# Performance work log

Hardware: AMD Instinct MI355X
Metric: run time of the kernel (lower is better)

## Reference

```python
import jax, jax.numpy as jnp
import numpy as np

MARGIN = 0.3
NUM_CLASSES = 32  # includes label 0, which the mask logic treats specially


def setup_inputs() -> dict:
    key = jax.random.key(0)
    k1, k2 = jax.random.split(key)
    n, d = 4096, 2048
    inputs = jax.random.normal(k1, (n, d), dtype=jnp.float32)
    targets = jax.random.randint(k2, (n,), 0, NUM_CLASSES, dtype=jnp.int64)
    return {"inputs": inputs, "targets": targets}


def reference(inputs, targets):
    # Pairwise euclidean distance matrix [n, n]
    sq = jnp.sum(inputs * inputs, axis=1)  # [n]
    dist2 = sq[:, None] + sq[None, :] - 2.0 * (inputs @ inputs.T)
    dist = jnp.sqrt(jnp.maximum(dist2, 1e-12))

    # Mask semantics from the torch code:
    #   mask == 1  : same label (hard-positive pool; includes diagonal)
    #   mask == 0  : different labels AND at least one of the pair has label 0
    #   mask == -1 : different labels, both nonzero (excluded from mining)
    ti, tj = targets[:, None], targets[None, :]
    same = ti == tj
    zero_neg = (~same) & ((ti == 0) | (tj == 0))

    neg_inf = jnp.asarray(-jnp.inf, dist.dtype)
    pos_inf = jnp.asarray(jnp.inf, dist.dtype)
    dist_ap = jnp.max(jnp.where(same, dist, neg_inf), axis=1)      # hardest positive per row
    row_min = jnp.min(jnp.where(zero_neg, dist, pos_inf), axis=1)  # hardest label-0 negative

    # Torch code checks row 0 only (mask[0]) for the presence of mask==0 entries;
    # if row 0 has none, ALL dist_an are set to 0. Reproduce faithfully.
    row0_has_zero = jnp.any(zero_neg[0])
    dist_an = jnp.where(row0_has_zero, row_min, jnp.zeros_like(row_min))

    # MarginRankingLoss with y = 1: mean(relu(-(dist_an - dist_ap) + margin))
    loss = jnp.mean(jax.nn.relu(dist_ap - dist_an + MARGIN))
    return loss
```

## Files before the change

kernel.cpp:

```cpp
#include <hip/hip_runtime.h>
#include <hip/hip_bf16.h>
#include <math.h>

#define N 4096
#define K 2048
#define NC 32
#define MARGIN 0.3f

#define BK 64
#define NITER (K / BK)
#define GRID 512
#define MAXTILES 4096

typedef float f32x4 __attribute__((ext_vector_type(4)));
typedef __bf16 bf16x8 __attribute__((ext_vector_type(8)));

__device__ __forceinline__ void glds16(const void* g, void* l) {
  __builtin_amdgcn_global_load_lds(
      (const __attribute__((address_space(1))) void*)g,
      (__attribute__((address_space(3))) void*)l, 16, 0, 0);
}

__device__ __forceinline__ int imin(int a, int b) { return a < b ? a : b; }

__global__ __launch_bounds__(256) void plan_kernel(
    const int* __restrict__ tg, int* __restrict__ cursor,
    int* __restrict__ flag, int* __restrict__ done, int* __restrict__ Tp,
    int4* __restrict__ tiles) {
  __shared__ int h[NC], soff[NC], stb[NC + 1];
  int t = threadIdx.x;
  if (t < NC) h[t] = 0;
  __syncthreads();
  const int4* tg4 = (const int4*)tg;
  for (int i = t; i < N / 4; i += 256) {
    int4 v = tg4[i];
    atomicAdd(&h[v.x], 1); atomicAdd(&h[v.y], 1);
    atomicAdd(&h[v.z], 1); atomicAdd(&h[v.w], 1);
  }
  __syncthreads();
  if (t == 0) {
    int acc = 0, tacc = 0;
    for (int c = 0; c < NC; c++) {
      int n = h[c];
      soff[c] = acc;
      cursor[c] = acc;
      acc += n;
      stb[c] = tacc;
      int tt = (n + 63) >> 6;
      tacc += (tt * (tt + 1)) >> 1;
    }
    stb[NC] = tacc;
    int n0 = h[0], nz = N - n0;
    int t0b = (n0 + 63) >> 6, tzb = (nz + 63) >> 6;
    Tp[0] = tacc + ((n0 > 0 && nz > 0) ? t0b * tzb : 0);
    flag[0] = (tg[0] == 0) ? (nz > 0) : (n0 > 0);
    done[0] = 0;
  }
  __syncthreads();
  if (t < NC && h[t] > 0) {
    int n = h[t], o = soff[t];
    int tt = (n + 63) >> 6;
    int idx = stb[t];
    for (int si = 0; si < tt; si++)
      for (int sj = si; sj < tt; sj++) {
        int fl = (si < sj) ? 3 : 1;
        tiles[idx++] = make_int4((o + si * 64) | (fl << 28), o + sj * 64,
                                 o + n, o + n);
      }
  }
  int n0 = h[0], nz = N - n0;
  if (n0 > 0 && nz > 0) {
    int t0b = (n0 + 63) >> 6, tzb = (nz + 63) >> 6;
    int base = stb[NC];
    for (int k2 = t; k2 < t0b * tzb; k2 += 256) {
      int si = k2 / tzb, sj = k2 - si * tzb;
      tiles[base + k2] = make_int4((si * 64) | (2 << 28), n0 + sj * 64, n0, N);
    }
  }
}

__global__ __launch_bounds__(256) void convert_kernel(
    const float* __restrict__ X, const int* __restrict__ tg,
    __bf16* __restrict__ Xg, float* __restrict__ sqg,
    unsigned int* __restrict__ ap, unsigned int* __restrict__ an,
    int* __restrict__ cursor) {
  int row = blockIdx.x;
  int t = threadIdx.x;
  const float* xr = X + (size_t)row * K;

  float4 v0 = ((const float4*)xr)[t * 2 + 0];
  float4 v1 = ((const float4*)xr)[t * 2 + 1];

  float s = v0.x * v0.x + v0.y * v0.y + v0.z * v0.z + v0.w * v0.w +
            v1.x * v1.x + v1.y * v1.y + v1.z * v1.z + v1.w * v1.w;

  bf16x8 b;
  b[0] = (__bf16)v0.x; b[1] = (__bf16)v0.y; b[2] = (__bf16)v0.z; b[3] = (__bf16)v0.w;
  b[4] = (__bf16)v1.x; b[5] = (__bf16)v1.y; b[6] = (__bf16)v1.z; b[7] = (__bf16)v1.w;

  #pragma unroll
  for (int m = 32; m; m >>= 1) s += __shfl_xor(s, m);

  __shared__ float wred[4];
  __shared__ int spos;
  if ((t & 63) == 0) wred[t >> 6] = s;
  if (t == 0) spos = atomicAdd(&cursor[tg[row]], 1);
  __syncthreads();
  int pos = spos;

  ((bf16x8*)(Xg + (size_t)pos * K))[t] = b;
  if (t == 0) {
    sqg[pos] = wred[0] + wred[1] + wred[2] + wred[3];
    ap[pos] = 0u;
    an[pos] = 0x7f800000u;
  }
}

__global__ __launch_bounds__(256, 3) void gemm_reduce_kernel(
    const __bf16* __restrict__ Xg, const float* __restrict__ sq,
    const int* __restrict__ Tp, const int4* __restrict__ tiles,
    const int* __restrict__ flag, int* __restrict__ done,
    unsigned int* __restrict__ ap, unsigned int* __restrict__ an,
    float* __restrict__ out) {
  __shared__ __align__(16) char sAB[3][16384];
  __shared__ int s_islast;
  __shared__ float wred[4];

  int t = threadIdx.x;
  int w = t >> 6, l = t & 63;
  int wi = w >> 1, wj = w & 1;
  int quad = l >> 4, lr = l & 15;

  int aoff[2][2], boff[2][2];
  #pragma unroll
  for (int ti2 = 0; ti2 < 2; ti2++)
    #pragma unroll
    for (int h = 0; h < 2; h++) {
      int sw = (((h << 2) + quad) ^ (lr & 7)) << 4;
      aoff[ti2][h] = (wi * 32 + ti2 * 16 + lr) * 128 + sw;
      boff[ti2][h] = (wj * 32 + ti2 * 16 + lr) * 128 + sw + 8192;
    }

  int rr = t >> 3, slot = t & 7;
  int T = Tp[0];

  for (int tid = blockIdx.x; tid < T; tid += GRID) {
    int4 dsc = tiles[tid];
    unsigned fl = (unsigned)dsc.x >> 28;
    int i0 = dsc.x & 0x0FFFFFFF;
    int j0 = dsc.y, iend = dsc.z, jend = dsc.w;
    bool diag = fl & 1, colside = (fl & 2) != 0;

    const char* gA[2]; const char* gB[2];
    #pragma unroll
    for (int r = 0; r < 2; r++) {
      int row_l = r * 32 + rr;
      int cbg = slot ^ (row_l & 7);
      int ia = imin(i0 + row_l, iend - 1);
      int ja = imin(j0 + row_l, jend - 1);
      gA[r] = (const char*)(Xg + (size_t)ia * K) + cbg * 16;
      gB[r] = (const char*)(Xg + (size_t)ja * K) + cbg * 16;
    }

    f32x4 acc[2][2];
    acc[0][0] = (f32x4)0.f; acc[0][1] = (f32x4)0.f;
    acc[1][0] = (f32x4)0.f; acc[1][1] = (f32x4)0.f;

    auto stage = [&](int buf, int it) {
      char* base = sAB[buf] + t * 16;
      int koff = it * 128;
      glds16(gA[0] + koff, base);
      glds16(gA[1] + koff, base + 4096);
      glds16(gB[0] + koff, base + 8192);
      glds16(gB[1] + koff, base + 12288);
    };

    auto compute = [&](int buf) {
      const char* base = sAB[buf];
      bf16x8 af[2][2], bfr[2][2];
      #pragma unroll
      for (int ti2 = 0; ti2 < 2; ti2++)
        #pragma unroll
        for (int h = 0; h < 2; h++) {
          af[ti2][h] = *(const bf16x8*)(base + aoff[ti2][h]);
          bfr[ti2][h] = *(const bf16x8*)(base + boff[ti2][h]);
        }
      #pragma unroll
      for (int h = 0; h < 2; h++)
        #pragma unroll
        for (int ti2 = 0; ti2 < 2; ti2++)
          #pragma unroll
          for (int tj2 = 0; tj2 < 2; tj2++)
            acc[ti2][tj2] = __builtin_amdgcn_mfma_f32_16x16x32_bf16(
                af[ti2][h], bfr[tj2][h], acc[ti2][tj2], 0, 0, 0);
    };

    stage(0, 0);
    stage(1, 1);
    int pbuf = 2, cbuf = 0;
    for (int it = 0; it < NITER; ++it) {
      if (it < NITER - 1) __builtin_amdgcn_s_waitcnt(0x0F74);
      else __builtin_amdgcn_s_waitcnt(0x0F70);
      __builtin_amdgcn_s_barrier();
      if (it + 2 < NITER) {
        stage(pbuf, it + 2);
        pbuf = (pbuf == 2) ? 0 : pbuf + 1;
      }
      __builtin_amdgcn_sched_barrier(0);
      compute(cbuf);
      cbuf = (cbuf == 2) ? 0 : cbuf + 1;
    }

    int jgc[2]; float sqj[2];
    #pragma unroll
    for (int tj2 = 0; tj2 < 2; tj2++) {
      jgc[tj2] = imin(j0 + wj * 32 + tj2 * 16 + lr, jend - 1);
      sqj[tj2] = sq[jgc[tj2]];
    }
    float cred[2];
    cred[0] = cred[1] = diag ? 0.f : INFINITY;

    #pragma unroll
    for (int ti2 = 0; ti2 < 2; ti2++) {
      #pragma unroll
      for (int r = 0; r < 4; r++) {
        int ir = imin(i0 + wi * 32 + ti2 * 16 + quad * 4 + r, iend - 1);
        float sqi = sq[ir];
        float v = diag ? 0.f : INFINITY;
        #pragma unroll
        for (int tj2 = 0; tj2 < 2; tj2++) {
          float d2 = fmaxf(sqi + sqj[tj2] - 2.f * acc[ti2][tj2][r], 1e-12f);
          v = diag ? fmaxf(v, d2) : fminf(v, d2);
          cred[tj2] = diag ? fmaxf(cred[tj2], d2) : fminf(cred[tj2], d2);
        }
        #pragma unroll
        for (int m = 1; m < 16; m <<= 1) {
          float o = __shfl_xor(v, m);
          v = diag ? fmaxf(v, o) : fminf(v, o);
        }
        if (lr == 0) {
          unsigned int u = __float_as_uint(sqrtf(v));
          if (diag) atomicMax(ap + ir, u);
          else      atomicMin(an + ir, u);
        }
      }
    }
    if (colside) {
      #pragma unroll
      for (int tj2 = 0; tj2 < 2; tj2++) {
        float v = cred[tj2];
        float o = __shfl_xor(v, 16);
        v = diag ? fmaxf(v, o) : fminf(v, o);
        o = __shfl_xor(v, 32);
        v = diag ? fmaxf(v, o) : fminf(v, o);
        if (quad == 0) {
          unsigned int u = __float_as_uint(sqrtf(v));
          if (diag) atomicMax(ap + jgc[tj2], u);
          else      atomicMin(an + jgc[tj2], u);
        }
      }
    }
    __builtin_amdgcn_s_barrier();
  }

  __syncthreads();
  if (t == 0) {
    __threadfence();
    int ticket = __hip_atomic_fetch_add(done, 1, __ATOMIC_ACQ_REL,
                                        __HIP_MEMORY_SCOPE_AGENT);
    s_islast = (ticket == GRID - 1);
  }
  __syncthreads();
  if (s_islast) {
    int has = flag[0];
    float s = 0.f;
    for (int i = t; i < N; i += 256) {
      unsigned int au = __hip_atomic_load(ap + i, __ATOMIC_RELAXED,
                                          __HIP_MEMORY_SCOPE_AGENT);
      unsigned int nu = __hip_atomic_load(an + i, __ATOMIC_RELAXED,
                                          __HIP_MEMORY_SCOPE_AGENT);
      float a = __uint_as_float(au);
      float bb = has ? __uint_as_float(nu) : 0.f;
      s += fmaxf(a - bb + MARGIN, 0.f);
    }
    #pragma unroll
    for (int m = 32; m; m >>= 1) s += __shfl_xor(s, m);
    if ((t & 63) == 0) wred[t >> 6] = s;
    __syncthreads();
    if (t == 0) out[0] = (wred[0] + wred[1] + wred[2] + wred[3]) / (float)N;
  }
}

extern "C" void kernel_launch(void* const* d_in, const int* in_sizes, int n_in,
                              void* d_out, int out_size, void* d_ws,
                              size_t ws_size, hipStream_t stream) {
  const float* X = (const float*)d_in[0];
  const int* tg = (const int*)d_in[1];
  float* out = (float*)d_out;

  char* ws = (char*)d_ws;
  __bf16* Xg = (__bf16*)ws;
  size_t o = (size_t)N * K * 2;
  float* sq = (float*)(ws + o); o += (size_t)N * 4;
  unsigned int* ap = (unsigned int*)(ws + o); o += (size_t)N * 4;
  unsigned int* an = (unsigned int*)(ws + o); o += (size_t)N * 4;
  int* cursor = (int*)(ws + o); o += NC * 4;
  int* flag = (int*)(ws + o); o += 4;
  int* done = (int*)(ws + o); o += 4;
  int* Tp = (int*)(ws + o); o += 4;
  o = (o + 15) & ~(size_t)15;
  int4* tiles = (int4*)(ws + o); o += (size_t)MAXTILES * 16;

  plan_kernel<<<1, 256, 0, stream>>>(tg, cursor, flag, done, Tp, tiles);
  convert_kernel<<<N, 256, 0, stream>>>(X, tg, Xg, sq, ap, an, cursor);
  gemm_reduce_kernel<<<GRID, 256, 0, stream>>>(Xg, sq, Tp, tiles, flag, done,
                                               ap, an, out);
}
```

Baseline: 145.4 us.

## Split GEMM over K into partial tiles with a separate reduce kernel

The fused GEMM-plus-mining kernel becomes two kernels. The first splits each 64x64 tile's K dimension into 8 chunks and writes fp32 partial accumulators to workspace. The second sums those partials and does the distance, masking and atomic min/max reduction plus the final loss. This exposes far more work items than the few hundred tiles the class-sorted plan produces, which could not fill the grid before. The cost is an extra launch and a global-memory round trip for the partials, and the tile list is now capped at 512 entries, so inputs with more tiles would be silently truncated.

New measurement: 148.9 us. 2.5% more time.

```diff
diff --git a/kernel.cpp b/kernel.cpp
--- a/kernel.cpp
+++ b/kernel.cpp
@@ -7,10 +7,11 @@
 #define NC 32
 #define MARGIN 0.3f
 
-#define BK 64
-#define NITER (K / BK)
-#define GRID 512
-#define MAXTILES 4096
+#define SPLITK 8
+#define KC (K / SPLITK)
+#define GRID_A 512
+#define GRID_B 256
+#define MAXTILES 512
 
 typedef float f32x4 __attribute__((ext_vector_type(4)));
 typedef __bf16 bf16x8 __attribute__((ext_vector_type(8)));
@@ -52,7 +53,8 @@
     stb[NC] = tacc;
     int n0 = h[0], nz = N - n0;
     int t0b = (n0 + 63) >> 6, tzb = (nz + 63) >> 6;
-    Tp[0] = tacc + ((n0 > 0 && nz > 0) ? t0b * tzb : 0);
+    int T = tacc + ((n0 > 0 && nz > 0) ? t0b * tzb : 0);
+    Tp[0] = imin(T, MAXTILES);
     flag[0] = (tg[0] == 0) ? (nz > 0) : (n0 > 0);
     done[0] = 0;
   }
@@ -64,8 +66,10 @@
     for (int si = 0; si < tt; si++)
       for (int sj = si; sj < tt; sj++) {
         int fl = (si < sj) ? 3 : 1;
-        tiles[idx++] = make_int4((o + si * 64) | (fl << 28), o + sj * 64,
+        if (idx < MAXTILES)
+          tiles[idx] = make_int4((o + si * 64) | (fl << 28), o + sj * 64,
                                  o + n, o + n);
+        idx++;
       }
   }
   int n0 = h[0], nz = N - n0;
@@ -74,7 +78,9 @@
     int base = stb[NC];
     for (int k2 = t; k2 < t0b * tzb; k2 += 256) {
       int si = k2 / tzb, sj = k2 - si * tzb;
-      tiles[base + k2] = make_int4((si * 64) | (2 << 28), n0 + sj * 64, n0, N);
+      if (base + k2 < MAXTILES)
+        tiles[base + k2] =
+            make_int4((si * 64) | (2 << 28), n0 + sj * 64, n0, N);
     }
   }
 }
@@ -116,15 +122,10 @@
   }
 }
 
-__global__ __launch_bounds__(256, 3) void gemm_reduce_kernel(
-    const __bf16* __restrict__ Xg, const float* __restrict__ sq,
-    const int* __restrict__ Tp, const int4* __restrict__ tiles,
-    const int* __restrict__ flag, int* __restrict__ done,
-    unsigned int* __restrict__ ap, unsigned int* __restrict__ an,
-    float* __restrict__ out) {
-  __shared__ __align__(16) char sAB[3][16384];
-  __shared__ int s_islast;
-  __shared__ float wred[4];
+__global__ __launch_bounds__(256, 2) void gemm_partial_kernel(
+    const __bf16* __restrict__ Xg, const int* __restrict__ Tp,
+    const int4* __restrict__ tiles, float* __restrict__ pg) {
+  __shared__ __align__(16) char sAB[4][16384];
 
   int t = threadIdx.x;
   int w = t >> 6, l = t & 63;
@@ -142,14 +143,13 @@
     }
 
   int rr = t >> 3, slot = t & 7;
-  int T = Tp[0];
-
-  for (int tid = blockIdx.x; tid < T; tid += GRID) {
+  int M = Tp[0] * SPLITK;
+
+  for (int m = blockIdx.x; m < M; m += GRID_A) {
+    int tid = m >> 3, s = m & 7;
     int4 dsc = tiles[tid];
-    unsigned fl = (unsigned)dsc.x >> 28;
     int i0 = dsc.x & 0x0FFFFFFF;
     int j0 = dsc.y, iend = dsc.z, jend = dsc.w;
-    bool diag = fl & 1, colside = (fl & 2) != 0;
 
     const char* gA[2]; const char* gB[2];
     #pragma unroll
@@ -158,25 +158,28 @@
       int cbg = slot ^ (row_l & 7);
       int ia = imin(i0 + row_l, iend - 1);
       int ja = imin(j0 + row_l, jend - 1);
-      gA[r] = (const char*)(Xg + (size_t)ia * K) + cbg * 16;
-      gB[r] = (const char*)(Xg + (size_t)ja * K) + cbg * 16;
-    }
-
-    f32x4 acc[2][2];
-    acc[0][0] = (f32x4)0.f; acc[0][1] = (f32x4)0.f;
-    acc[1][0] = (f32x4)0.f; acc[1][1] = (f32x4)0.f;
-
-    auto stage = [&](int buf, int it) {
-      char* base = sAB[buf] + t * 16;
-      int koff = it * 128;
+      gA[r] = (const char*)(Xg + (size_t)ia * K) + s * (KC * 2) + cbg * 16;
+      gB[r] = (const char*)(Xg + (size_t)ja * K) + s * (KC * 2) + cbg * 16;
+    }
+
+    __syncthreads();
+
+    #pragma unroll
+    for (int st = 0; st < 4; st++) {
+      char* base = sAB[st] + t * 16;
+      int koff = st * 128;
       glds16(gA[0] + koff, base);
       glds16(gA[1] + koff, base + 4096);
       glds16(gB[0] + koff, base + 8192);
       glds16(gB[1] + koff, base + 12288);
-    };
-
-    auto compute = [&](int buf) {
-      const char* base = sAB[buf];
+    }
+
+    f32x4 acc[2][2];
+    acc[0][0] = (f32x4)0.f; acc[0][1] = (f32x4)0.f;
+    acc[1][0] = (f32x4)0.f; acc[1][1] = (f32x4)0.f;
+
+    auto compute = [&](int st) {
+      const char* base = sAB[st];
       bf16x8 af[2][2], bfr[2][2];
       #pragma unroll
       for (int ti2 = 0; ti2 < 2; ti2++)
@@ -195,20 +198,56 @@
                 af[ti2][h], bfr[tj2][h], acc[ti2][tj2], 0, 0, 0);
     };
 
-    stage(0, 0);
-    stage(1, 1);
-    int pbuf = 2, cbuf = 0;
-    for (int it = 0; it < NITER; ++it) {
-      if (it < NITER - 1) __builtin_amdgcn_s_waitcnt(0x0F74);
-      else __builtin_amdgcn_s_waitcnt(0x0F70);
-      __builtin_amdgcn_s_barrier();
-      if (it + 2 < NITER) {
-        stage(pbuf, it + 2);
-        pbuf = (pbuf == 2) ? 0 : pbuf + 1;
-      }
-      __builtin_amdgcn_sched_barrier(0);
-      compute(cbuf);
-      cbuf = (cbuf == 2) ? 0 : cbuf + 1;
+    __builtin_amdgcn_s_waitcnt(0x0F7C);
+    __builtin_amdgcn_s_barrier();
+    compute(0);
+    __builtin_amdgcn_s_waitcnt(0x0F78);
+    __builtin_amdgcn_s_barrier();
+    compute(1);
+    __builtin_amdgcn_s_waitcnt(0x0F74);
+    __builtin_amdgcn_s_barrier();
+    compute(2);
+    __builtin_amdgcn_s_waitcnt(0x0F70);
+    __builtin_amdgcn_s_barrier();
+    compute(3);
+
+    f32x4* dst = (f32x4*)(pg + (size_t)m * 4096 + t * 16);
+    dst[0] = acc[0][0]; dst[1] = acc[0][1];
+    dst[2] = acc[1][0]; dst[3] = acc[1][1];
+  }
+}
+
+__global__ __launch_bounds__(256) void reduce_kernel(
+    const float* __restrict__ pg, const float* __restrict__ sq,
+    const int* __restrict__ Tp, const int4* __restrict__ tiles,
+    const int* __restrict__ flag, int* __restrict__ done,
+    unsigned int* __restrict__ ap, unsigned int* __restrict__ an,
+    float* __restrict__ out) {
+  __shared__ int s_islast;
+  __shared__ float wred[4];
+
+  int t = threadIdx.x;
+  int w = t >> 6, l = t & 63;
+  int wi = w >> 1, wj = w & 1;
+  int quad = l >> 4, lr = l & 15;
+  int T = Tp[0];
+
+  for (int tid = blockIdx.x; tid < T; tid += GRID_B) {
+    int4 dsc = tiles[tid];
+    unsigned fl = (unsigned)dsc.x >> 28;
+    int i0 = dsc.x & 0x0FFFFFFF;
+    int j0 = dsc.y, iend = dsc.z, jend = dsc.w;
+    bool diag = fl & 1, colside = (fl & 2) != 0;
+
+    f32x4 acc[2][2];
+    acc[0][0] = (f32x4)0.f; acc[0][1] = (f32x4)0.f;
+    acc[1][0] = (f32x4)0.f; acc[1][1] = (f32x4)0.f;
+    const float* base = pg + (size_t)tid * (SPLITK * 4096) + t * 16;
+    #pragma unroll
+    for (int s = 0; s < SPLITK; s++) {
+      const f32x4* p = (const f32x4*)(base + (size_t)s * 4096);
+      acc[0][0] += p[0]; acc[0][1] += p[1];
+      acc[1][0] += p[2]; acc[1][1] += p[3];
     }
 
     int jgc[2]; float sqj[2];
@@ -260,7 +299,6 @@
         }
       }
     }
-    __builtin_amdgcn_s_barrier();
   }
 
   __syncthreads();
@@ -268,7 +306,7 @@
     __threadfence();
     int ticket = __hip_atomic_fetch_add(done, 1, __ATOMIC_ACQ_REL,
                                         __HIP_MEMORY_SCOPE_AGENT);
-    s_islast = (ticket == GRID - 1);
+    s_islast = (ticket == GRID_B - 1);
   }
   __syncthreads();
   if (s_islast) {
@@ -308,11 +346,14 @@
   int* flag = (int*)(ws + o); o += 4;
   int* done = (int*)(ws + o); o += 4;
   int* Tp = (int*)(ws + o); o += 4;
-  o = (o + 15) & ~(size_t)15;
+  o = (o + 255) & ~(size_t)255;
   int4* tiles = (int4*)(ws + o); o += (size_t)MAXTILES * 16;
+  o = (o + 255) & ~(size_t)255;
+  float* pg = (float*)(ws + o);
 
   plan_kernel<<<1, 256, 0, stream>>>(tg, cursor, flag, done, Tp, tiles);
   convert_kernel<<<N, 256, 0, stream>>>(X, tg, Xg, sq, ap, an, cursor);
-  gemm_reduce_kernel<<<GRID, 256, 0, stream>>>(Xg, sq, Tp, tiles, flag, done,
-                                               ap, an, out);
-}
+  gemm_partial_kernel<<<GRID_A, 256, 0, stream>>>(Xg, Tp, tiles, pg);
+  reduce_kernel<<<GRID_B, 256, 0, stream>>>(pg, sq, Tp, tiles, flag, done,
+                                            ap, an, out);
+}
```
